# Performance work log

Hardware: AMD Instinct MI355X
Metric: run time of the kernel (lower is better)

Reference implementation:

```python
import jax, jax.numpy as jnp
import numpy as np

N = 16384      # total nodes (8 graphs x 2048)
E = 262144     # edges (avg degree 16)
TW = 25        # time_window
H = 128        # hidden_features
POS_DIM = 2
NB = 8         # number of graphs in batch
L = 6          # hidden_layer
DT = 0.01
EPS = 1e-5
MSG_IN = 2 * H + TW + POS_DIM + 1   # 284 (actual message concat width)
UPD_IN = H + H + 1                  # 257
EMB_IN = TW + POS_DIM + 1           # 28


def _lin(key, fan_in, fan_out):
    return jax.random.normal(key, (fan_in, fan_out), jnp.float32) / np.sqrt(fan_in)


def setup_inputs() -> dict:
    key = jax.random.key(0)
    ks = jax.random.split(key, 24)
    inp = {}
    inp["u"] = jax.random.normal(ks[0], (N, TW), jnp.float32)
    inp["pos"] = jax.random.uniform(ks[1], (N, 1 + POS_DIM), jnp.float32)
    inp["edge_index"] = jax.random.randint(ks[2], (2, E), 0, N)
    inp["batch"] = jnp.sort(jax.random.randint(ks[3], (N,), 0, NB))
    # embedding MLP
    inp["emb_W1"] = _lin(ks[4], EMB_IN, H); inp["emb_b1"] = jnp.zeros((H,), jnp.float32)
    inp["emb_W2"] = _lin(ks[5], H, H);      inp["emb_b2"] = jnp.zeros((H,), jnp.float32)
    # 6 GNN layers (stacked)
    inp["msg_W1"] = jax.vmap(lambda k: _lin(k, MSG_IN, H))(jax.random.split(ks[6], L))
    inp["msg_b1"] = jnp.zeros((L, H), jnp.float32)
    inp["msg_W2"] = jax.vmap(lambda k: _lin(k, H, H))(jax.random.split(ks[7], L))
    inp["msg_b2"] = jnp.zeros((L, H), jnp.float32)
    inp["upd_W1"] = jax.vmap(lambda k: _lin(k, UPD_IN, H))(jax.random.split(ks[8], L))
    inp["upd_b1"] = jnp.zeros((L, H), jnp.float32)
    inp["upd_W2"] = jax.vmap(lambda k: _lin(k, H, H))(jax.random.split(ks[9], L))
    inp["upd_b2"] = jnp.zeros((L, H), jnp.float32)
    # output CNN: Conv1d(1,8,15,s4) -> Conv1d(8,4,10,s2) -> Conv1d(4,1,10,s1)
    inp["conv1_W"] = jax.random.normal(ks[10], (8, 1, 15), jnp.float32) / np.sqrt(15)
    inp["conv1_b"] = jnp.zeros((8,), jnp.float32)
    inp["conv2_W"] = jax.random.normal(ks[11], (4, 8, 10), jnp.float32) / np.sqrt(80)
    inp["conv2_b"] = jnp.zeros((4,), jnp.float32)
    inp["conv3_W"] = jax.random.normal(ks[12], (1, 4, 10), jnp.float32) / np.sqrt(40)
    inp["conv3_b"] = jnp.zeros((1,), jnp.float32)
    return inp


def _mlp2(x, W1, b1, W2, b2):
    return jax.nn.relu(jax.nn.relu(x @ W1 + b1) @ W2 + b2)


def _instance_norm(h, batch):
    # PyG InstanceNorm (affine=False): per-graph, per-channel normalization
    cnt = jax.ops.segment_sum(jnp.ones((h.shape[0], 1), h.dtype), batch, NB)
    cnt = jnp.maximum(cnt, 1.0)
    mean = jax.ops.segment_sum(h, batch, NB) / cnt
    meansq = jax.ops.segment_sum(h * h, batch, NB) / cnt
    var = jnp.maximum(meansq - mean * mean, 0.0)
    return (h - mean[batch]) * jax.lax.rsqrt(var[batch] + EPS)


def _gnn_layer(h, u, pos_sp, variables, src, dst, batch,
               mW1, mb1, mW2, mb2, uW1, ub1, uW2, ub2):
    # message: gather endpoints, concat, 2-layer ReLU MLP  [E, MSG_IN] -> [E, H]
    m_in = jnp.concatenate([h[dst], h[src], u[dst] - u[src],
                            pos_sp[dst] - pos_sp[src], variables[dst]], axis=-1)
    msg = _mlp2(m_in, mW1, mb1, mW2, mb2)
    # mean-scatter aggregation onto target nodes
    deg = jax.ops.segment_sum(jnp.ones((src.shape[0], 1), h.dtype), dst, N)
    agg = jax.ops.segment_sum(msg, dst, N) / jnp.maximum(deg, 1.0)
    # node update MLP + residual (in_features == out_features)
    upd = _mlp2(jnp.concatenate([h, agg, variables], axis=-1), uW1, ub1, uW2, ub2)
    return _instance_norm(h + upd, batch)


def _conv1d(x, W, b, stride):
    # x: [N, C_in, L], W: [C_out, C_in, K]
    y = jax.lax.conv_general_dilated(x, W, (stride,), 'VALID',
                                     dimension_numbers=('NCH', 'OIH', 'NCH'))
    return y + b[None, :, None]


def reference(u, pos, edge_index, batch,
              emb_W1, emb_b1, emb_W2, emb_b2,
              msg_W1, msg_b1, msg_W2, msg_b2,
              upd_W1, upd_b1, upd_W2, upd_b2,
              conv1_W, conv1_b, conv2_W, conv2_b, conv3_W, conv3_b):
    variables = pos[:, 0:1]          # time variable
    pos_sp = pos[:, 1:1 + POS_DIM]   # spatial coords
    node_input = jnp.concatenate([u, pos_sp[:, 0:1], pos_sp[:, 1:2], variables], axis=-1)
    h = _mlp2(node_input, emb_W1, emb_b1, emb_W2, emb_b2)  # [N, H]
    src, dst = edge_index[0], edge_index[1]  # PyG: row 0 = source (j), row 1 = target (i)
    for l in range(L):
        h = _gnn_layer(h, u, pos_sp, variables, src, dst, batch,
                       msg_W1[l], msg_b1[l], msg_W2[l], msg_b2[l],
                       upd_W1[l], upd_b1[l], upd_W2[l], upd_b2[l])
    # output CNN: [N,1,128] -> [N,1,1]
    y = jax.nn.relu(_conv1d(h[:, None, :], conv1_W, conv1_b, 4))
    y = jax.nn.relu(_conv1d(y, conv2_W, conv2_b, 2))
    diff = _conv1d(y, conv3_W, conv3_b, 1)[:, 0, :]        # [N, 1]
    dt = jnp.cumsum(jnp.full((1, TW), DT, jnp.float32), axis=1)
    return u[:, -1:] + dt * diff                            # [N, TW]
```

## Files before the change

### kernel.cpp

```cpp
#include <hip/hip_runtime.h>

#define NN 16384
#define NE 262144
#define TWC 25
#define HC 128
#define NBC 8
#define LC 6
#define MINC 284
#define UINC 257
#define EINC 28
#define EPSC 1e-5
#define DTC 0.01f
#define SP 65

typedef float v2f __attribute__((ext_vector_type(2)));

#define KSTEPP(ACCF, WV, ROW, KW)                                        \
  do {                                                                   \
    v2f a01_ = {sm[(ROW) * SP + e0 + 0], sm[(ROW) * SP + e0 + 1]};       \
    v2f a23_ = {sm[(ROW) * SP + e0 + 2], sm[(ROW) * SP + e0 + 3]};       \
    float4 w0_ = WV[(KW) * 32 + jg * 2];                                 \
    float4 w1_ = WV[(KW) * 32 + jg * 2 + 1];                             \
    float wv_[8] = {w0_.x, w0_.y, w0_.z, w0_.w,                          \
                    w1_.x, w1_.y, w1_.z, w1_.w};                         \
    _Pragma("unroll") for (int j_ = 0; j_ < 8; ++j_) {                   \
      v2f ws_ = {wv_[j_], wv_[j_]};                                      \
      ACCF[0][j_] = __builtin_elementwise_fma(a01_, ws_, ACCF[0][j_]);   \
      ACCF[1][j_] = __builtin_elementwise_fma(a23_, ws_, ACCF[1][j_]);   \
    }                                                                    \
  } while (0)

#define KSTEPPN(ACCF, WV, ROW, KW)                                       \
  do {                                                                   \
    v2f a01_ = {sm[(ROW) * SP + e0 + 0], sm[(ROW) * SP + e0 + 1]};       \
    v2f a23_ = {sm[(ROW) * SP + e0 + 2], sm[(ROW) * SP + e0 + 3]};       \
    a01_ = -a01_; a23_ = -a23_;                                          \
    float4 w0_ = WV[(KW) * 32 + jg * 2];                                 \
    float4 w1_ = WV[(KW) * 32 + jg * 2 + 1];                             \
    float wv_[8] = {w0_.x, w0_.y, w0_.z, w0_.w,                          \
                    w1_.x, w1_.y, w1_.z, w1_.w};                         \
    _Pragma("unroll") for (int j_ = 0; j_ < 8; ++j_) {                   \
      v2f ws_ = {wv_[j_], wv_[j_]};                                      \
      ACCF[0][j_] = __builtin_elementwise_fma(a01_, ws_, ACCF[0][j_]);   \
      ACCF[1][j_] = __builtin_elementwise_fma(a23_, ws_, ACCF[1][j_]);   \
    }                                                                    \
  } while (0)

#define FLUSH32P(ACCD, ACCF)                                             \
  do {                                                                   \
    _Pragma("unroll") for (int i_ = 0; i_ < 4; ++i_)                     \
      _Pragma("unroll") for (int j_ = 0; j_ < 8; ++j_)                   \
        ACCD[i_][j_] += (double)ACCF[i_ >> 1][j_][i_ & 1];               \
    _Pragma("unroll") for (int i_ = 0; i_ < 2; ++i_)                     \
      _Pragma("unroll") for (int j_ = 0; j_ < 8; ++j_)                   \
        ACCF[i_][j_] = (v2f){0.f, 0.f};                                  \
  } while (0)

#define ACC_INIT(ACCD, ACCF, BV)                                         \
  do {                                                                   \
    _Pragma("unroll") for (int j_ = 0; j_ < 8; ++j_) {                   \
      double bv_ = (BV);                                                 \
      _Pragma("unroll") for (int i_ = 0; i_ < 4; ++i_) ACCD[i_][j_] = bv_; \
      ACCF[0][j_] = (v2f){0.f, 0.f};                                     \
      ACCF[1][j_] = (v2f){0.f, 0.f};                                     \
    }                                                                    \
  } while (0)


__global__ __launch_bounds__(256) void k_cnt(const int* __restrict__ dst,
                                             int* __restrict__ cnt) {
  int e = blockIdx.x * 256 + threadIdx.x;
  if (e < NE) atomicAdd(&cnt[dst[e]], 1);
}

__global__ __launch_bounds__(256) void k_scan(const int* __restrict__ cnt,
                                              int* __restrict__ rowptr,
                                              int* __restrict__ fill) {
  __shared__ int part[256];
  int t = threadIdx.x;
  int s = 0;
  for (int i = 0; i < 64; ++i) s += cnt[t * 64 + i];
  part[t] = s;
  __syncthreads();
  if (t == 0) {
    int r = 0;
    for (int i = 0; i < 256; ++i) { int v = part[i]; part[i] = r; r += v; }
  }
  __syncthreads();
  int r = part[t];
  for (int i = 0; i < 64; ++i) {
    int n = t * 64 + i;
    rowptr[n] = r;
    fill[n] = r;
    r += cnt[n];
  }
  if (t == 255) rowptr[NN] = r;
}

__global__ __launch_bounds__(256) void k_scatter(const int* __restrict__ src,
                                                 const int* __restrict__ dst,
                                                 int* __restrict__ fill,
                                                 int* __restrict__ srcS,
                                                 int* __restrict__ dstS) {
  int e = blockIdx.x * 256 + threadIdx.x;
  if (e < NE) {
    int d = dst[e];
    int p = atomicAdd(&fill[d], 1);
    srcS[p] = src[e];
    dstS[p] = d;
  }
}

__global__ __launch_bounds__(256) void k_rdeg(const int* __restrict__ rowptr,
                                              float* __restrict__ rdeg) {
  int n = blockIdx.x * 256 + threadIdx.x;
  if (n < NN) {
    int c = rowptr[n + 1] - rowptr[n];
    rdeg[n] = 1.0f / (float)max(c, 1);
  }
}

__global__ __launch_bounds__(256) void k_cntb(const int* __restrict__ batch,
                                              float* __restrict__ cntb) {
  int n = blockIdx.x * 256 + threadIdx.x;
  int b = (n < NN) ? batch[n] : -1;
#pragma unroll
  for (int bb = 0; bb < NBC; ++bb) {
    unsigned long long m = __ballot(b == bb);
    if ((threadIdx.x & 63) == 0 && m != 0ULL)
      atomicAdd(&cntb[bb], (float)__popcll(m));
  }
}

__global__ __launch_bounds__(256) void k_emb(
    const float* __restrict__ u, const float* __restrict__ pos,
    const float* __restrict__ W1, const float* __restrict__ b1,
    const float* __restrict__ W2, const float* __restrict__ b2,
    float* __restrict__ h) {
  __shared__ float sin_[2][EINC];
  __shared__ float shid[2][HC];
  int n0 = blockIdx.x * 2;
  int t = threadIdx.x;
  if (t < 2 * EINC) {
    int e = t / EINC, c = t - e * EINC;
    int n = n0 + e;
    float v;
    if (c < TWC) v = u[n * TWC + c];
    else if (c == TWC) v = pos[n * 3 + 1];
    else if (c == TWC + 1) v = pos[n * 3 + 2];
    else v = pos[n * 3 + 0];
    sin_[e][c] = v;
  }
  __syncthreads();
  int e = t >> 7, j = t & 127;
  double acc = (double)b1[j];
  for (int k = 0; k < EINC; ++k)
    acc = fma((double)sin_[e][k], (double)W1[k * HC + j], acc);
  shid[e][j] = fmaxf((float)acc, 0.f);
  __syncthreads();
  double acc2 = (double)b2[j];
  for (int k = 0; k < HC; ++k)
    acc2 = fma((double)shid[e][k], (double)W2[k * HC + j], acc2);
  h[(n0 + e) * HC + j] = fmaxf((float)acc2, 0.f);
}

__global__ __launch_bounds__(256) void k_node(
    const float* __restrict__ h, const float* __restrict__ u,
    const float* __restrict__ pos, const float* __restrict__ W1,
    const float* __restrict__ b1, float* __restrict__ Dv,
    float* __restrict__ Sv) {
  __shared__ float sm[156 * SP];
  const int t = threadIdx.x;
  const int n_base = blockIdx.x * 64;
  const int eg = t >> 4, jg = t & 15;
  const int e0 = eg * 4, j0 = jg * 8;
  const int half = t >> 7, col = t & 127;

  for (int it = 0; it < 32; ++it) {
    int e = 2 * it + half;
    sm[col * SP + e] = h[(n_base + e) * HC + col];
  }
  for (int idx = t; idx < 64 * 28; idx += 256) {
    int e = idx / 28, c = idx - e * 28;
    int n = n_base + e;
    float v;
    if (c < TWC) v = u[n * TWC + c];
    else if (c == TWC) v = pos[n * 3 + 1];
    else if (c == TWC + 1) v = pos[n * 3 + 2];
    else v = pos[n * 3 + 0];
    sm[(128 + c) * SP + e] = v;
  }
  __syncthreads();

  const float4* W1v = (const float4*)W1;
  v2f accf[2][8];
  double accd[4][8];

  ACC_INIT(accd, accf, (double)b1[j0 + j_]);
  for (int kc = 0; kc < 128; kc += 32) {
#pragma unroll
    for (int kk = 0; kk < 32; ++kk) KSTEPP(accf, W1v, kc + kk, kc + kk);
    FLUSH32P(accd, accf);
  }
#pragma unroll
  for (int kk = 0; kk < 28; ++kk) KSTEPP(accf, W1v, 128 + kk, 256 + kk);
  FLUSH32P(accd, accf);
#pragma unroll
  for (int i = 0; i < 4; ++i) {
    int n = n_base + e0 + i;
#pragma unroll
    for (int jj = 0; jj < 8; ++jj)
      Dv[n * HC + j0 + jj] = (float)accd[i][jj];
  }

  ACC_INIT(accd, accf, 0.0);
  for (int kc = 0; kc < 128; kc += 32) {
#pragma unroll
    for (int kk = 0; kk < 32; ++kk) KSTEPP(accf, W1v, kc + kk, 128 + kc + kk);
    FLUSH32P(accd, accf);
  }
#pragma unroll
  for (int kk = 0; kk < 27; ++kk) KSTEPPN(accf, W1v, 128 + kk, 256 + kk);
  FLUSH32P(accd, accf);
#pragma unroll
  for (int i = 0; i < 4; ++i) {
    int n = n_base + e0 + i;
#pragma unroll
    for (int jj = 0; jj < 8; ++jj)
      Sv[n * HC + j0 + jj] = (float)accd[i][jj];
  }
}

__global__ __launch_bounds__(256) void k_msg(
    const float* __restrict__ Dv, const float* __restrict__ Sv,
    const int* __restrict__ srcS, const int* __restrict__ dstS,
    const float* __restrict__ W2, const float* __restrict__ b2,
    float* __restrict__ agg) {
  __shared__ float sm[128 * SP];
  const int t = threadIdx.x;
  const int e_base = blockIdx.x * 64;
  const int eg = t >> 4, jg = t & 15;
  const int e0 = eg * 4, j0 = jg * 8;
  const int half = t >> 7, col = t & 127;

  if (t < 64) {
    sm[t * SP + 64] = __int_as_float(dstS[e_base + t]);
    sm[(64 + t) * SP + 64] = __int_as_float(srcS[e_base + t]);
  }
  __syncthreads();

  for (int it = 0; it < 32; ++it) {
    int e = 2 * it + half;
    int nd = __float_as_int(sm[e * SP + 64]);
    int ns = __float_as_int(sm[(64 + e) * SP + 64]);
    sm[col * SP + e] = fmaxf(Dv[nd * HC + col] + Sv[ns * HC + col], 0.f);
  }
  __syncthreads();

  v2f accf[2][8];
  double accd[4][8];
  ACC_INIT(accd, accf, (double)b2[j0 + j_]);

  const float4* W2v = (const float4*)W2;
  for (int kc = 0; kc < 128; kc += 32) {
#pragma unroll
    for (int kk = 0; kk < 32; ++kk) KSTEPP(accf, W2v, kc + kk, kc + kk);
    FLUSH32P(accd, accf);
  }
  __syncthreads();

#pragma unroll
  for (int jj = 0; jj < 8; ++jj) {
#pragma unroll
    for (int i = 0; i < 4; ++i)
      sm[(j0 + jj) * SP + e0 + i] = fmaxf((float)accd[i][jj], 0.f);
  }
  __syncthreads();

  {
    int j = t & 127;
    int ebeg = (t >> 7) * 32;
    float s = 0.f;
    int cur = __float_as_int(sm[ebeg * SP + 64]);
    for (int e = ebeg; e < ebeg + 32; ++e) {
      int d = __float_as_int(sm[e * SP + 64]);
      if (d != cur) {
        atomicAdd(&agg[cur * HC + j], s);
        s = 0.f;
        cur = d;
      }
      s += sm[j * SP + e];
    }
    atomicAdd(&agg[cur * HC + j], s);
  }
}

__global__ __launch_bounds__(256) void k_upd(
    const float* __restrict__ h, const float* __restrict__ pos,
    const float* __restrict__ agg, const float* __restrict__ rdeg,
    const float* __restrict__ W1, const float* __restrict__ b1,
    const float* __restrict__ W2, const float* __restrict__ b2,
    float* __restrict__ hn) {
  __shared__ float sm[129 * SP];
  const int t = threadIdx.x;
  const int n_base = blockIdx.x * 64;
  const int eg = t >> 4, jg = t & 15;
  const int e0 = eg * 4, j0 = jg * 8;
  const int half = t >> 7, col = t & 127;

  v2f accf[2][8];
  double accd[4][8];
  ACC_INIT(accd, accf, (double)b1[j0 + j_]);

  for (int it = 0; it < 32; ++it) {
    int e = 2 * it + half;
    sm[col * SP + e] = h[(n_base + e) * HC + col];
  }
  __syncthreads();

  const float4* W1v = (const float4*)W1;
  for (int kc = 0; kc < 128; kc += 32) {
#pragma unroll
    for (int kk = 0; kk < 32; ++kk) KSTEPP(accf, W1v, kc + kk, kc + kk);
    FLUSH32P(accd, accf);
  }
  __syncthreads();

  for (int it = 0; it < 32; ++it) {
    int e = 2 * it + half;
    int n = n_base + e;
    sm[col * SP + e] = agg[n * HC + col] * rdeg[n];
  }
  if (t < 64) sm[128 * SP + t] = pos[(n_base + t) * 3 + 0];
  __syncthreads();

  for (int kc = 0; kc < 128; kc += 32) {
#pragma unroll
    for (int kk = 0; kk < 32; ++kk) KSTEPP(accf, W1v, kc + kk, 128 + kc + kk);
    FLUSH32P(accd, accf);
  }
  KSTEPP(accf, W1v, 128, 256);
  FLUSH32P(accd, accf);
  __syncthreads();

#pragma unroll
  for (int jj = 0; jj < 8; ++jj) {
#pragma unroll
    for (int i = 0; i < 4; ++i)
      sm[(j0 + jj) * SP + e0 + i] = fmaxf((float)accd[i][jj], 0.f);
  }
  __syncthreads();

  ACC_INIT(accd, accf, (double)b2[j0 + j_]);
  const float4* W2v = (const float4*)W2;
  for (int kc = 0; kc < 128; kc += 32) {
#pragma unroll
    for (int kk = 0; kk < 32; ++kk) KSTEPP(accf, W2v, kc + kk, kc + kk);
    FLUSH32P(accd, accf);
  }

#pragma unroll
  for (int i = 0; i < 4; ++i) {
    int n = n_base + e0 + i;
#pragma unroll
    for (int jj = 0; jj < 8; ++jj) {
      int j = j0 + jj;
      hn[n * HC + j] = h[n * HC + j] + fmaxf((float)accd[i][jj], 0.f);
    }
  }
}

__global__ __launch_bounds__(256) void k_stats(const float* __restrict__ hn,
                                               const int* __restrict__ batch,
                                               double* __restrict__ stats) {
  int n0 = blockIdx.x * 32;
  int ch = threadIdx.x & 127;
  int rh = threadIdx.x >> 7;
  double s = 0.0, ss = 0.0;
  int cur = batch[n0 + rh];
  for (int r = rh; r < 32; r += 2) {
    int n = n0 + r;
    int b = batch[n];
    double v = (double)hn[n * HC + ch];
    if (b != cur) {
      atomicAdd(&stats[cur * HC + ch], s);
      atomicAdd(&stats[NBC * HC + cur * HC + ch], ss);
      s = 0.0; ss = 0.0; cur = b;
    }
    s += v;
    ss += v * v;
  }
  atomicAdd(&stats[cur * HC + ch], s);
  atomicAdd(&stats[NBC * HC + cur * HC + ch], ss);
}

__global__ __launch_bounds__(256) void k_norm(
    const float* __restrict__ hn, const int* __restrict__ batch,
    const double* __restrict__ stats, const float* __restrict__ cntb,
    float* __restrict__ hout) {
  int idx = blockIdx.x * 256 + threadIdx.x;
  int n = idx >> 7, ch = idx & 127;
  int b = batch[n];
  double c = fmax((double)cntb[b], 1.0);
  double mean = stats[b * HC + ch] / c;
  double ms = stats[NBC * HC + b * HC + ch] / c;
  double var = fmax(ms - mean * mean, 0.0);
  hout[idx] = (float)(((double)hn[idx] - mean) / sqrt(var + EPSC));
}

__global__ __launch_bounds__(64) void k_head(
    const float* __restrict__ h, const float* __restrict__ u,
    const float* __restrict__ c1W, const float* __restrict__ c1b,
    const float* __restrict__ c2W, const float* __restrict__ c2b,
    const float* __restrict__ c3W, const float* __restrict__ c3b,
    float* __restrict__ out) {
  __shared__ float hr[128];
  __shared__ float y1[8 * 29];
  __shared__ float y2[4 * 10];
  __shared__ float dv;
  int n = blockIdx.x, t = threadIdx.x;
  hr[t] = h[n * HC + t];
  hr[t + 64] = h[n * HC + 64 + t];
  __syncthreads();
  for (int idx = t; idx < 8 * 29; idx += 64) {
    int o = idx / 29, p = idx - o * 29;
    float acc = c1b[o];
    for (int q = 0; q < 15; ++q) acc = fmaf(hr[p * 4 + q], c1W[o * 15 + q], acc);
    y1[o * 29 + p] = fmaxf(acc, 0.f);
  }
  __syncthreads();
  if (t < 40) {
    int o = t / 10, p = t - o * 10;
    float acc = c2b[o];
    for (int i = 0; i < 8; ++i)
      for (int q = 0; q < 10; ++q)
        acc = fmaf(y1[i * 29 + p * 2 + q], c2W[o * 80 + i * 10 + q], acc);
    y2[o * 10 + p] = fmaxf(acc, 0.f);
  }
  __syncthreads();
  if (t == 0) {
    float acc = c3b[0];
    for (int i = 0; i < 4; ++i)
      for (int q = 0; q < 10; ++q)
        acc = fmaf(y2[i * 10 + q], c3W[i * 10 + q], acc);
    dv = acc;
  }
  __syncthreads();
  if (t < TWC) out[n * TWC + t] = u[n * TWC + 24] + DTC * (float)(t + 1) * dv;
}

extern "C" void kernel_launch(void* const* d_in, const int* in_sizes, int n_in,
                              void* d_out, int out_size, void* d_ws,
                              size_t ws_size, hipStream_t stream) {
  const float* u = (const float*)d_in[0];
  const float* pos = (const float*)d_in[1];
  const int* ei = (const int*)d_in[2];
  const int* batch = (const int*)d_in[3];
  const float* eW1 = (const float*)d_in[4];
  const float* eb1 = (const float*)d_in[5];
  const float* eW2 = (const float*)d_in[6];
  const float* eb2 = (const float*)d_in[7];
  const float* mW1 = (const float*)d_in[8];
  const float* mb1 = (const float*)d_in[9];
  const float* mW2 = (const float*)d_in[10];
  const float* mb2 = (const float*)d_in[11];
  const float* uW1 = (const float*)d_in[12];
  const float* ub1 = (const float*)d_in[13];
  const float* uW2 = (const float*)d_in[14];
  const float* ub2 = (const float*)d_in[15];
  const float* c1W = (const float*)d_in[16];
  const float* c1b = (const float*)d_in[17];
  const float* c2W = (const float*)d_in[18];
  const float* c2b = (const float*)d_in[19];
  const float* c3W = (const float*)d_in[20];
  const float* c3b = (const float*)d_in[21];
  float* out = (float*)d_out;

  const int* srcI = ei;
  const int* dstI = ei + NE;

  double* statsd = (double*)d_ws;
  float* h = (float*)(statsd + 2 * NBC * HC);
  float* Sv = h + NN * HC;
  float* agg = Sv + NN * HC;
  float* Dhn = agg + NN * HC;
  float* rdeg = Dhn + NN * HC;
  float* cntb = rdeg + NN;
  int* cnt = (int*)(cntb + NBC);
  int* rowptr = cnt + NN;
  int* fill = rowptr + NN + 1;
  int* srcS = fill + NN;
  int* dstS = srcS + NE;

  hipMemsetAsync(cnt, 0, NN * sizeof(int), stream);
  hipMemsetAsync(cntb, 0, NBC * sizeof(float), stream);
  k_cnt<<<NE / 256, 256, 0, stream>>>(dstI, cnt);
  k_scan<<<1, 256, 0, stream>>>(cnt, rowptr, fill);
  k_scatter<<<NE / 256, 256, 0, stream>>>(srcI, dstI, fill, srcS, dstS);
  k_rdeg<<<NN / 256, 256, 0, stream>>>(rowptr, rdeg);
  k_cntb<<<NN / 256, 256, 0, stream>>>(batch, cntb);
  k_emb<<<NN / 2, 256, 0, stream>>>(u, pos, eW1, eb1, eW2, eb2, h);

  for (int l = 0; l < LC; ++l) {
    hipMemsetAsync(agg, 0, (size_t)NN * HC * sizeof(float), stream);
    hipMemsetAsync(statsd, 0, 2 * NBC * HC * sizeof(double), stream);
    k_node<<<NN / 64, 256, 0, stream>>>(
        h, u, pos, mW1 + (size_t)l * MINC * HC, mb1 + l * HC, Dhn, Sv);
    k_msg<<<NE / 64, 256, 0, stream>>>(Dhn, Sv, srcS, dstS,
                                       mW2 + (size_t)l * HC * HC, mb2 + l * HC,
                                       agg);
    k_upd<<<NN / 64, 256, 0, stream>>>(h, pos, agg, rdeg,
                                       uW1 + (size_t)l * UINC * HC, ub1 + l * HC,
                                       uW2 + (size_t)l * HC * HC, ub2 + l * HC,
                                       Dhn);
    k_stats<<<NN / 32, 256, 0, stream>>>(Dhn, batch, statsd);
    k_norm<<<NN * HC / 256, 256, 0, stream>>>(Dhn, batch, statsd, cntb, h);
  }
  k_head<<<NN, 64, 0, stream>>>(h, u, c1W, c1b, c2W, c2b, c3W, c3b, out);
}
```

Before: 2.253 ms.

## Halve per-block row tile to 32 and remap thread-to-output mapping

```diff
diff --git a/kernel.cpp b/kernel.cpp
--- a/kernel.cpp
+++ b/kernel.cpp
@@ -11,58 +11,53 @@
 #define EINC 28
 #define EPSC 1e-5
 #define DTC 0.01f
-#define SP 65
+#define SP 33
 
 typedef float v2f __attribute__((ext_vector_type(2)));
 
 #define KSTEPP(ACCF, WV, ROW, KW)                                        \
   do {                                                                   \
-    v2f a01_ = {sm[(ROW) * SP + e0 + 0], sm[(ROW) * SP + e0 + 1]};       \
-    v2f a23_ = {sm[(ROW) * SP + e0 + 2], sm[(ROW) * SP + e0 + 3]};       \
+    v2f a_ = {sm[(ROW) * SP + e0], sm[(ROW) * SP + e0 + 1]};             \
     float4 w0_ = WV[(KW) * 32 + jg * 2];                                 \
     float4 w1_ = WV[(KW) * 32 + jg * 2 + 1];                             \
     float wv_[8] = {w0_.x, w0_.y, w0_.z, w0_.w,                          \
                     w1_.x, w1_.y, w1_.z, w1_.w};                         \
     _Pragma("unroll") for (int j_ = 0; j_ < 8; ++j_) {                   \
       v2f ws_ = {wv_[j_], wv_[j_]};                                      \
-      ACCF[0][j_] = __builtin_elementwise_fma(a01_, ws_, ACCF[0][j_]);   \
-      ACCF[1][j_] = __builtin_elementwise_fma(a23_, ws_, ACCF[1][j_]);   \
+      ACCF[j_] = __builtin_elementwise_fma(a_, ws_, ACCF[j_]);           \
     }                                                                    \
   } while (0)
 
 #define KSTEPPN(ACCF, WV, ROW, KW)                                       \
   do {                                                                   \
-    v2f a01_ = {sm[(ROW) * SP + e0 + 0], sm[(ROW) * SP + e0 + 1]};       \
-    v2f a23_ = {sm[(ROW) * SP + e0 + 2], sm[(ROW) * SP + e0 + 3]};       \
-    a01_ = -a01_; a23_ = -a23_;                                          \
+    v2f a_ = {sm[(ROW) * SP + e0], sm[(ROW) * SP + e0 + 1]};             \
+    a_ = -a_;                                                            \
     float4 w0_ = WV[(KW) * 32 + jg * 2];                                 \
     float4 w1_ = WV[(KW) * 32 + jg * 2 + 1];                             \
     float wv_[8] = {w0_.x, w0_.y, w0_.z, w0_.w,                          \
                     w1_.x, w1_.y, w1_.z, w1_.w};                         \
     _Pragma("unroll") for (int j_ = 0; j_ < 8; ++j_) {                   \
       v2f ws_ = {wv_[j_], wv_[j_]};                                      \
-      ACCF[0][j_] = __builtin_elementwise_fma(a01_, ws_, ACCF[0][j_]);   \
-      ACCF[1][j_] = __builtin_elementwise_fma(a23_, ws_, ACCF[1][j_]);   \
+      ACCF[j_] = __builtin_elementwise_fma(a_, ws_, ACCF[j_]);           \
     }                                                                    \
   } while (0)
 
 #define FLUSH32P(ACCD, ACCF)                                             \
   do {                                                                   \
-    _Pragma("unroll") for (int i_ = 0; i_ < 4; ++i_)                     \
-      _Pragma("unroll") for (int j_ = 0; j_ < 8; ++j_)                   \
-        ACCD[i_][j_] += (double)ACCF[i_ >> 1][j_][i_ & 1];               \
-    _Pragma("unroll") for (int i_ = 0; i_ < 2; ++i_)                     \
-      _Pragma("unroll") for (int j_ = 0; j_ < 8; ++j_)                   \
-        ACCF[i_][j_] = (v2f){0.f, 0.f};                                  \
+    _Pragma("unroll") for (int j_ = 0; j_ < 8; ++j_) {                   \
+      ACCD[0][j_] += (double)ACCF[j_][0];                                \
+      ACCD[1][j_] += (double)ACCF[j_][1];                                \
+      ACCF[j_] = (v2f){0.f, 0.f};                                       \
+    }                                                                    \
   } while (0)
 
 #define ACC_INIT(ACCD, ACCF, BV)                                         \
   do {                                                                   \
     _Pragma("unroll") for (int j_ = 0; j_ < 8; ++j_) {                   \
       double bv_ = (BV);                                                 \
-      _Pragma("unroll") for (int i_ = 0; i_ < 4; ++i_) ACCD[i_][j_] = bv_; \
-      ACCF[0][j_] = (v2f){0.f, 0.f};                                     \
-      ACCF[1][j_] = (v2f){0.f, 0.f};                                     \
+      ACCD[0][j_] = bv_;                                                 \
+      ACCD[1][j_] = bv_;                                                 \
+      ACCF[j_] = (v2f){0.f, 0.f};                                       \
     }                                                                    \
   } while (0)
 
@@ -171,16 +166,16 @@
     float* __restrict__ Sv) {
   __shared__ float sm[156 * SP];
   const int t = threadIdx.x;
-  const int n_base = blockIdx.x * 64;
-  const int eg = t >> 4, jg = t & 15;
-  const int e0 = eg * 4, j0 = jg * 8;
+  const int n_base = blockIdx.x * 32;
+  const int eg = t & 15, jg = t >> 4;
+  const int e0 = eg * 2, j0 = jg * 8;
   const int half = t >> 7, col = t & 127;
 
-  for (int it = 0; it < 32; ++it) {
+  for (int it = 0; it < 16; ++it) {
     int e = 2 * it + half;
     sm[col * SP + e] = h[(n_base + e) * HC + col];
   }
-  for (int idx = t; idx < 64 * 28; idx += 256) {
+  for (int idx = t; idx < 32 * 28; idx += 256) {
     int e = idx / 28, c = idx - e * 28;
     int n = n_base + e;
     float v;
@@ -193,8 +188,8 @@
   __syncthreads();
 
   const float4* W1v = (const float4*)W1;
-  v2f accf[2][8];
-  double accd[4][8];
+  v2f accf[8];
+  double accd[2][8];
 
   ACC_INIT(accd, accf, (double)b1[j0 + j_]);
   for (int kc = 0; kc < 128; kc += 32) {
@@ -206,7 +201,7 @@
   for (int kk = 0; kk < 28; ++kk) KSTEPP(accf, W1v, 128 + kk, 256 + kk);
   FLUSH32P(accd, accf);
 #pragma unroll
-  for (int i = 0; i < 4; ++i) {
+  for (int i = 0; i < 2; ++i) {
     int n = n_base + e0 + i;
 #pragma unroll
     for (int jj = 0; jj < 8; ++jj)
@@ -223,7 +218,7 @@
   for (int kk = 0; kk < 27; ++kk) KSTEPPN(accf, W1v, 128 + kk, 256 + kk);
   FLUSH32P(accd, accf);
 #pragma unroll
-  for (int i = 0; i < 4; ++i) {
+  for (int i = 0; i < 2; ++i) {
     int n = n_base + e0 + i;
 #pragma unroll
     for (int jj = 0; jj < 8; ++jj)
@@ -231,34 +226,34 @@
   }
 }
 
-__global__ __launch_bounds__(256) void k_msg(
+__global__ __launch_bounds__(256, 8) void k_msg(
     const float* __restrict__ Dv, const float* __restrict__ Sv,
     const int* __restrict__ srcS, const int* __restrict__ dstS,
     const float* __restrict__ W2, const float* __restrict__ b2,
     float* __restrict__ agg) {
   __shared__ float sm[128 * SP];
   const int t = threadIdx.x;
-  const int e_base = blockIdx.x * 64;
-  const int eg = t >> 4, jg = t & 15;
-  const int e0 = eg * 4, j0 = jg * 8;
+  const int e_base = blockIdx.x * 32;
+  const int eg = t & 15, jg = t >> 4;
+  const int e0 = eg * 2, j0 = jg * 8;
   const int half = t >> 7, col = t & 127;
 
-  if (t < 64) {
-    sm[t * SP + 64] = __int_as_float(dstS[e_base + t]);
-    sm[(64 + t) * SP + 64] = __int_as_float(srcS[e_base + t]);
-  }
-  __syncthreads();
-
-  for (int it = 0; it < 32; ++it) {
+  if (t < 32) {
+    sm[t * SP + 32] = __int_as_float(dstS[e_base + t]);
+    sm[(32 + t) * SP + 32] = __int_as_float(srcS[e_base + t]);
+  }
+  __syncthreads();
+
+  for (int it = 0; it < 16; ++it) {
     int e = 2 * it + half;
-    int nd = __float_as_int(sm[e * SP + 64]);
-    int ns = __float_as_int(sm[(64 + e) * SP + 64]);
+    int nd = __float_as_int(sm[e * SP + 32]);
+    int ns = __float_as_int(sm[(32 + e) * SP + 32]);
     sm[col * SP + e] = fmaxf(Dv[nd * HC + col] + Sv[ns * HC + col], 0.f);
   }
   __syncthreads();
 
-  v2f accf[2][8];
-  double accd[4][8];
+  v2f accf[8];
+  double accd[2][8];
   ACC_INIT(accd, accf, (double)b2[j0 + j_]);
 
   const float4* W2v = (const float4*)W2;
@@ -272,18 +267,18 @@
 #pragma unroll
   for (int jj = 0; jj < 8; ++jj) {
 #pragma unroll
-    for (int i = 0; i < 4; ++i)
+    for (int i = 0; i < 2; ++i)
       sm[(j0 + jj) * SP + e0 + i] = fmaxf((float)accd[i][jj], 0.f);
   }
   __syncthreads();
 
   {
     int j = t & 127;
-    int ebeg = (t >> 7) * 32;
+    int ebeg = (t >> 7) * 16;
     float s = 0.f;
-    int cur = __float_as_int(sm[ebeg * SP + 64]);
-    for (int e = ebeg; e < ebeg + 32; ++e) {
-      int d = __float_as_int(sm[e * SP + 64]);
+    int cur = __float_as_int(sm[ebeg * SP + 32]);
+    for (int e = ebeg; e < ebeg + 16; ++e) {
+      int d = __float_as_int(sm[e * SP + 32]);
       if (d != cur) {
         atomicAdd(&agg[cur * HC + j], s);
         s = 0.f;
@@ -303,16 +298,16 @@
     float* __restrict__ hn) {
   __shared__ float sm[129 * SP];
   const int t = threadIdx.x;
-  const int n_base = blockIdx.x * 64;
-  const int eg = t >> 4, jg = t & 15;
-  const int e0 = eg * 4, j0 = jg * 8;
+  const int n_base = blockIdx.x * 32;
+  const int eg = t & 15, jg = t >> 4;
+  const int e0 = eg * 2, j0 = jg * 8;
   const int half = t >> 7, col = t & 127;
 
-  v2f accf[2][8];
-  double accd[4][8];
+  v2f accf[8];
+  double accd[2][8];
   ACC_INIT(accd, accf, (double)b1[j0 + j_]);
 
-  for (int it = 0; it < 32; ++it) {
+  for (int it = 0; it < 16; ++it) {
     int e = 2 * it + half;
     sm[col * SP + e] = h[(n_base + e) * HC + col];
   }
@@ -326,12 +321,12 @@
   }
   __syncthreads();
 
-  for (int it = 0; it < 32; ++it) {
+  for (int it = 0; it < 16; ++it) {
     int e = 2 * it + half;
     int n = n_base + e;
     sm[col * SP + e] = agg[n * HC + col] * rdeg[n];
   }
-  if (t < 64) sm[128 * SP + t] = pos[(n_base + t) * 3 + 0];
+  if (t < 32) sm[128 * SP + t] = pos[(n_base + t) * 3 + 0];
   __syncthreads();
 
   for (int kc = 0; kc < 128; kc += 32) {
@@ -346,7 +341,7 @@
 #pragma unroll
   for (int jj = 0; jj < 8; ++jj) {
 #pragma unroll
-    for (int i = 0; i < 4; ++i)
+    for (int i = 0; i < 2; ++i)
       sm[(j0 + jj) * SP + e0 + i] = fmaxf((float)accd[i][jj], 0.f);
   }
   __syncthreads();
@@ -360,7 +355,7 @@
   }
 
 #pragma unroll
-  for (int i = 0; i < 4; ++i) {
+  for (int i = 0; i < 2; ++i) {
     int n = n_base + e0 + i;
 #pragma unroll
     for (int jj = 0; jj < 8; ++jj) {
@@ -504,12 +499,12 @@
   for (int l = 0; l < LC; ++l) {
     hipMemsetAsync(agg, 0, (size_t)NN * HC * sizeof(float), stream);
     hipMemsetAsync(statsd, 0, 2 * NBC * HC * sizeof(double), stream);
-    k_node<<<NN / 64, 256, 0, stream>>>(
+    k_node<<<NN / 32, 256, 0, stream>>>(
         h, u, pos, mW1 + (size_t)l * MINC * HC, mb1 + l * HC, Dhn, Sv);
-    k_msg<<<NE / 64, 256, 0, stream>>>(Dhn, Sv, srcS, dstS,
+    k_msg<<<NE / 32, 256, 0, stream>>>(Dhn, Sv, srcS, dstS,
                                        mW2 + (size_t)l * HC * HC, mb2 + l * HC,
                                        agg);
-    k_upd<<<NN / 64, 256, 0, stream>>>(h, pos, agg, rdeg,
+    k_upd<<<NN / 32, 256, 0, stream>>>(h, pos, agg, rdeg,
                                        uW1 + (size_t)l * UINC * HC, ub1 + l * HC,
                                        uW2 + (size_t)l * HC * HC, ub2 + l * HC,
                                        Dhn);
```

Result: slower. 3.115 ms (+38.2%).

## Halve k_msg shared memory by processing hidden channels in two halves

Applied to the files above, without the earlier changes.

```diff
diff --git a/kernel.cpp b/kernel.cpp
--- a/kernel.cpp
+++ b/kernel.cpp
@@ -231,67 +231,105 @@
   }
 }
 
-__global__ __launch_bounds__(256) void k_msg(
+__global__ __launch_bounds__(256, 8) void k_msg(
     const float* __restrict__ Dv, const float* __restrict__ Sv,
     const int* __restrict__ srcS, const int* __restrict__ dstS,
     const float* __restrict__ W2, const float* __restrict__ b2,
     float* __restrict__ agg) {
-  __shared__ float sm[128 * SP];
+  __shared__ float sm[64 * SP];
+  __shared__ int sdst[64];
+  __shared__ int ssrc[64];
   const int t = threadIdx.x;
-  const int e_base = blockIdx.x * 64;
+  const int bid = blockIdx.x;
+  const int e_base = ((bid & 7) * 512 + (bid >> 3)) * 64;
   const int eg = t >> 4, jg = t & 15;
   const int e0 = eg * 4, j0 = jg * 8;
-  const int half = t >> 7, col = t & 127;
+  const int sc = t & 63, sg = t >> 6;
 
   if (t < 64) {
-    sm[t * SP + 64] = __int_as_float(dstS[e_base + t]);
-    sm[(64 + t) * SP + 64] = __int_as_float(srcS[e_base + t]);
-  }
-  __syncthreads();
-
-  for (int it = 0; it < 32; ++it) {
-    int e = 2 * it + half;
-    int nd = __float_as_int(sm[e * SP + 64]);
-    int ns = __float_as_int(sm[(64 + e) * SP + 64]);
-    sm[col * SP + e] = fmaxf(Dv[nd * HC + col] + Sv[ns * HC + col], 0.f);
+    sdst[t] = dstS[e_base + t];
+    ssrc[t] = srcS[e_base + t];
   }
   __syncthreads();
 
   v2f accf[2][8];
   double accd[4][8];
   ACC_INIT(accd, accf, (double)b2[j0 + j_]);
-
   const float4* W2v = (const float4*)W2;
-  for (int kc = 0; kc < 128; kc += 32) {
+
+  for (int it = 0; it < 16; ++it) {
+    int e = sg * 16 + it;
+    int nd = sdst[e], ns = ssrc[e];
+    sm[sc * SP + e] = fmaxf(Dv[nd * HC + sc] + Sv[ns * HC + sc], 0.f);
+  }
+  __syncthreads();
+  for (int kc = 0; kc < 64; kc += 32) {
 #pragma unroll
     for (int kk = 0; kk < 32; ++kk) KSTEPP(accf, W2v, kc + kk, kc + kk);
     FLUSH32P(accd, accf);
   }
   __syncthreads();
 
-#pragma unroll
-  for (int jj = 0; jj < 8; ++jj) {
-#pragma unroll
-    for (int i = 0; i < 4; ++i)
-      sm[(j0 + jj) * SP + e0 + i] = fmaxf((float)accd[i][jj], 0.f);
-  }
-  __syncthreads();
-
+  for (int it = 0; it < 16; ++it) {
+    int e = sg * 16 + it;
+    int nd = sdst[e], ns = ssrc[e];
+    sm[sc * SP + e] = fmaxf(Dv[nd * HC + 64 + sc] + Sv[ns * HC + 64 + sc], 0.f);
+  }
+  __syncthreads();
+  for (int kc = 0; kc < 64; kc += 32) {
+#pragma unroll
+    for (int kk = 0; kk < 32; ++kk) KSTEPP(accf, W2v, kc + kk, 64 + kc + kk);
+    FLUSH32P(accd, accf);
+  }
+  __syncthreads();
+
+  if (jg < 8) {
+#pragma unroll
+    for (int jj = 0; jj < 8; ++jj)
+#pragma unroll
+      for (int i = 0; i < 4; ++i)
+        sm[(j0 + jj) * SP + e0 + i] = fmaxf((float)accd[i][jj], 0.f);
+  }
+  __syncthreads();
   {
-    int j = t & 127;
-    int ebeg = (t >> 7) * 32;
+    int ch = t & 63, sb = (t >> 6) * 16;
     float s = 0.f;
-    int cur = __float_as_int(sm[ebeg * SP + 64]);
-    for (int e = ebeg; e < ebeg + 32; ++e) {
-      int d = __float_as_int(sm[e * SP + 64]);
+    int cur = sdst[sb];
+    for (int e = sb; e < sb + 16; ++e) {
+      int d = sdst[e];
       if (d != cur) {
-        atomicAdd(&agg[cur * HC + j], s);
+        atomicAdd(&agg[cur * HC + ch], s);
         s = 0.f;
         cur = d;
       }
-      s += sm[j * SP + e];
+      s += sm[ch * SP + e];
     }
-    atomicAdd(&agg[cur * HC + j], s);
+    atomicAdd(&agg[cur * HC + ch], s);
+  }
+  __syncthreads();
+
+  if (jg >= 8) {
+#pragma unroll
+    for (int jj = 0; jj < 8; ++jj)
+#pragma unroll
+      for (int i = 0; i < 4; ++i)
+        sm[(j0 - 64 + jj) * SP + e0 + i] = fmaxf((float)accd[i][jj], 0.f);
+  }
+  __syncthreads();
+  {
+    int ch = t & 63, sb = (t >> 6) * 16;
+    float s = 0.f;
+    int cur = sdst[sb];
+    for (int e = sb; e < sb + 16; ++e) {
+      int d = sdst[e];
+      if (d != cur) {
+        atomicAdd(&agg[cur * HC + 64 + ch], s);
+        s = 0.f;
+        cur = d;
+      }
+      s += sm[ch * SP + e];
+    }
+    atomicAdd(&agg[cur * HC + 64 + ch], s);
   }
 }
 
```

After: 3.684 ms. 1.63x slower.

## Split node GEMM across grid, remap msg blocks, fuse stats into update kernel

Applied to the files above, without the earlier changes.

```diff
diff --git a/kernel.cpp b/kernel.cpp
--- a/kernel.cpp
+++ b/kernel.cpp
@@ -172,6 +172,7 @@
   __shared__ float sm[156 * SP];
   const int t = threadIdx.x;
   const int n_base = blockIdx.x * 64;
+  const int isS = blockIdx.y;
   const int eg = t >> 4, jg = t & 15;
   const int e0 = eg * 4, j0 = jg * 8;
   const int half = t >> 7, col = t & 127;
@@ -195,39 +196,30 @@
   const float4* W1v = (const float4*)W1;
   v2f accf[2][8];
   double accd[4][8];
-
-  ACC_INIT(accd, accf, (double)b1[j0 + j_]);
+  ACC_INIT(accd, accf, isS ? 0.0 : (double)b1[j0 + j_]);
+
+  const int wb = isS ? 128 : 0;
   for (int kc = 0; kc < 128; kc += 32) {
 #pragma unroll
-    for (int kk = 0; kk < 32; ++kk) KSTEPP(accf, W1v, kc + kk, kc + kk);
+    for (int kk = 0; kk < 32; ++kk) KSTEPP(accf, W1v, kc + kk, wb + kc + kk);
     FLUSH32P(accd, accf);
   }
-#pragma unroll
-  for (int kk = 0; kk < 28; ++kk) KSTEPP(accf, W1v, 128 + kk, 256 + kk);
+  if (!isS) {
+#pragma unroll
+    for (int kk = 0; kk < 28; ++kk) KSTEPP(accf, W1v, 128 + kk, 256 + kk);
+  } else {
+#pragma unroll
+    for (int kk = 0; kk < 27; ++kk) KSTEPPN(accf, W1v, 128 + kk, 256 + kk);
+  }
   FLUSH32P(accd, accf);
+
+  float* outp = isS ? Sv : Dv;
 #pragma unroll
   for (int i = 0; i < 4; ++i) {
     int n = n_base + e0 + i;
 #pragma unroll
     for (int jj = 0; jj < 8; ++jj)
-      Dv[n * HC + j0 + jj] = (float)accd[i][jj];
-  }
-
-  ACC_INIT(accd, accf, 0.0);
-  for (int kc = 0; kc < 128; kc += 32) {
-#pragma unroll
-    for (int kk = 0; kk < 32; ++kk) KSTEPP(accf, W1v, kc + kk, 128 + kc + kk);
-    FLUSH32P(accd, accf);
-  }
-#pragma unroll
-  for (int kk = 0; kk < 27; ++kk) KSTEPPN(accf, W1v, 128 + kk, 256 + kk);
-  FLUSH32P(accd, accf);
-#pragma unroll
-  for (int i = 0; i < 4; ++i) {
-    int n = n_base + e0 + i;
-#pragma unroll
-    for (int jj = 0; jj < 8; ++jj)
-      Sv[n * HC + j0 + jj] = (float)accd[i][jj];
+      outp[n * HC + j0 + jj] = (float)accd[i][jj];
   }
 }
 
@@ -238,7 +230,8 @@
     float* __restrict__ agg) {
   __shared__ float sm[128 * SP];
   const int t = threadIdx.x;
-  const int e_base = blockIdx.x * 64;
+  const int bid = blockIdx.x;
+  const int e_base = ((bid & 7) * 512 + (bid >> 3)) * 64;
   const int eg = t >> 4, jg = t & 15;
   const int e0 = eg * 4, j0 = jg * 8;
   const int half = t >> 7, col = t & 127;
@@ -298,10 +291,12 @@
 __global__ __launch_bounds__(256) void k_upd(
     const float* __restrict__ h, const float* __restrict__ pos,
     const float* __restrict__ agg, const float* __restrict__ rdeg,
-    const float* __restrict__ W1, const float* __restrict__ b1,
-    const float* __restrict__ W2, const float* __restrict__ b2,
-    float* __restrict__ hn) {
+    const int* __restrict__ batch, const float* __restrict__ W1,
+    const float* __restrict__ b1, const float* __restrict__ W2,
+    const float* __restrict__ b2, float* __restrict__ hn,
+    double* __restrict__ stats) {
   __shared__ float sm[129 * SP];
+  __shared__ int sbat[64];
   const int t = threadIdx.x;
   const int n_base = blockIdx.x * 64;
   const int eg = t >> 4, jg = t & 15;
@@ -358,6 +353,7 @@
     for (int kk = 0; kk < 32; ++kk) KSTEPP(accf, W2v, kc + kk, kc + kk);
     FLUSH32P(accd, accf);
   }
+  __syncthreads();
 
 #pragma unroll
   for (int i = 0; i < 4; ++i) {
@@ -365,33 +361,32 @@
 #pragma unroll
     for (int jj = 0; jj < 8; ++jj) {
       int j = j0 + jj;
-      hn[n * HC + j] = h[n * HC + j] + fmaxf((float)accd[i][jj], 0.f);
+      float v = h[n * HC + j] + fmaxf((float)accd[i][jj], 0.f);
+      hn[n * HC + j] = v;
+      sm[j * SP + e0 + i] = v;
     }
   }
-}
-
-__global__ __launch_bounds__(256) void k_stats(const float* __restrict__ hn,
-                                               const int* __restrict__ batch,
-                                               double* __restrict__ stats) {
-  int n0 = blockIdx.x * 32;
-  int ch = threadIdx.x & 127;
-  int rh = threadIdx.x >> 7;
-  double s = 0.0, ss = 0.0;
-  int cur = batch[n0 + rh];
-  for (int r = rh; r < 32; r += 2) {
-    int n = n0 + r;
-    int b = batch[n];
-    double v = (double)hn[n * HC + ch];
-    if (b != cur) {
-      atomicAdd(&stats[cur * HC + ch], s);
-      atomicAdd(&stats[NBC * HC + cur * HC + ch], ss);
-      s = 0.0; ss = 0.0; cur = b;
+  if (t < 64) sbat[t] = batch[n_base + t];
+  __syncthreads();
+
+  {
+    int ch = t & 127, rh = t >> 7;
+    double s = 0.0, ss = 0.0;
+    int cur = sbat[rh];
+    for (int e = rh; e < 64; e += 2) {
+      int b = sbat[e];
+      double v = (double)sm[ch * SP + e];
+      if (b != cur) {
+        atomicAdd(&stats[cur * HC + ch], s);
+        atomicAdd(&stats[NBC * HC + cur * HC + ch], ss);
+        s = 0.0; ss = 0.0; cur = b;
+      }
+      s += v;
+      ss += v * v;
     }
-    s += v;
-    ss += v * v;
-  }
-  atomicAdd(&stats[cur * HC + ch], s);
-  atomicAdd(&stats[NBC * HC + cur * HC + ch], ss);
+    atomicAdd(&stats[cur * HC + ch], s);
+    atomicAdd(&stats[NBC * HC + cur * HC + ch], ss);
+  }
 }
 
 __global__ __launch_bounds__(256) void k_norm(
@@ -504,16 +499,15 @@
   for (int l = 0; l < LC; ++l) {
     hipMemsetAsync(agg, 0, (size_t)NN * HC * sizeof(float), stream);
     hipMemsetAsync(statsd, 0, 2 * NBC * HC * sizeof(double), stream);
-    k_node<<<NN / 64, 256, 0, stream>>>(
+    k_node<<<dim3(NN / 64, 2), 256, 0, stream>>>(
         h, u, pos, mW1 + (size_t)l * MINC * HC, mb1 + l * HC, Dhn, Sv);
     k_msg<<<NE / 64, 256, 0, stream>>>(Dhn, Sv, srcS, dstS,
                                        mW2 + (size_t)l * HC * HC, mb2 + l * HC,
                                        agg);
-    k_upd<<<NN / 64, 256, 0, stream>>>(h, pos, agg, rdeg,
+    k_upd<<<NN / 64, 256, 0, stream>>>(h, pos, agg, rdeg, batch,
                                        uW1 + (size_t)l * UINC * HC, ub1 + l * HC,
                                        uW2 + (size_t)l * HC * HC, ub2 + l * HC,
-                                       Dhn);
-    k_stats<<<NN / 32, 256, 0, stream>>>(Dhn, batch, statsd);
+                                       Dhn, statsd);
     k_norm<<<NN * HC / 256, 256, 0, stream>>>(Dhn, batch, statsd, cntb, h);
   }
   k_head<<<NN, 64, 0, stream>>>(h, u, c1W, c1b, c2W, c2b, c3W, c3b, out);
```

After: 2.203 ms. 2.2% less time.
